# Optimization experiments

Measured on AMD Instinct MI355X. Metric: run time of the kernel, lower is better.

Reference implementation:

```python
import jax, jax.numpy as jnp
import numpy as np

N, E = 20000, 100000          # nodes, edges
H = 64                        # node_hidden_dim (== node_input_dim)
EIN, EH = 16, 128             # edge_input_dim, edge_hidden_dim
STEPS = 3                     # num_steps


def setup_inputs() -> dict:
    key = jax.random.key(0)
    ks = jax.random.split(key, 10)
    s = 0.05
    return {
        "node_features": jax.random.normal(ks[0], (N, H), jnp.float32),
        "edge_attr": jax.random.normal(ks[1], (E, EIN), jnp.float32),
        "edge_index": jax.random.randint(ks[2], (2, E), 0, N),
        # mp_input: Linear(H, H)
        "mp_w": jax.random.normal(ks[3], (H, H), jnp.float32) * s,
        "mp_b": jnp.zeros((H,), jnp.float32),
        # message_layer: Linear(2H, H)
        "msg_w": jax.random.normal(ks[4], (H, 2 * H), jnp.float32) * s,
        "msg_b": jnp.zeros((H,), jnp.float32),
        # edge network: Linear(EIN, EH) -> ReLU -> Linear(EH, H*H)
        "e1_w": jax.random.normal(ks[5], (EH, EIN), jnp.float32) * s,
        "e1_b": jnp.zeros((EH,), jnp.float32),
        "e2_w": jax.random.normal(ks[6], (H * H, EH), jnp.float32) * s,
        "e2_b": jnp.zeros((H * H,), jnp.float32),
        # NNConv root weight and bias
        "root": jax.random.normal(ks[7], (H, H), jnp.float32) * s,
        "conv_b": jnp.zeros((H,), jnp.float32),
    }


def reference(node_features, edge_attr, edge_index,
              mp_w, mp_b, msg_w, msg_b,
              e1_w, e1_b, e2_w, e2_b, root, conv_b):
    src, dst = edge_index[0], edge_index[1]
    out = jax.nn.relu(node_features @ mp_w.T + mp_b)  # [N, H]
    # Edge-conditioned weight matrices; edge_attr is constant across steps so
    # the edge MLP output is identical each step -> compute once (same math).
    W_e = (jax.nn.relu(edge_attr @ e1_w.T + e1_b) @ e2_w.T + e2_b).reshape(E, H, H)
    for _ in range(STEPS):
        # gather src features, per-edge matmul, scatter-add to dst
        msgs = jnp.einsum('ei,eio->eo', out[src], W_e)          # [E, H]
        agg = jax.ops.segment_sum(msgs, dst, num_segments=N)    # [N, H]
        m = jax.nn.relu(agg + out @ root + conv_b)              # NNConv + ReLU
        out = jnp.concatenate([m, out], axis=1) @ msg_w.T + msg_b
    return out + node_features
```

## Files before the change

kernel.cpp:

```cpp
#include <hip/hip_runtime.h>

#define N_ 20000
#define E_ 100000

typedef __attribute__((ext_vector_type(8))) short short8;
typedef __attribute__((ext_vector_type(8))) unsigned short ushort8;
typedef __attribute__((ext_vector_type(4))) float f32x4;

__device__ __forceinline__ unsigned short f2bf(float f) {
  union { float f; unsigned u; } v; v.f = f;
  unsigned r = v.u + 0x7fffu + ((v.u >> 16) & 1u);
  return (unsigned short)(r >> 16);
}
__device__ __forceinline__ float bf2f(unsigned short h) {
  union { unsigned u; float f; } v; v.u = ((unsigned)h) << 16;
  return v.f;
}

__global__ __launch_bounds__(256) void k_h2(const float* __restrict__ ea,
                                            const float* __restrict__ e1w,
                                            const float* __restrict__ e1b,
                                            unsigned short* __restrict__ h2) {
  int id = blockIdx.x * 256 + threadIdx.x;
  int e = id >> 7, k = id & 127;
  if (e >= E_) return;
  const float4* ar = (const float4*)(ea + e * 16);
  const float4* wr = (const float4*)(e1w + k * 16);
  float acc = e1b[k];
#pragma unroll
  for (int q = 0; q < 4; ++q) {
    float4 a = ar[q], w = wr[q];
    acc += a.x * w.x + a.y * w.y + a.z * w.z + a.w * w.w;
  }
  h2[id] = f2bf(fmaxf(acc, 0.f));
}

__global__ __launch_bounds__(256) void k_prep_bf(const float* __restrict__ e2w,
                                                 unsigned short* __restrict__ Bf) {
  int tid = blockIdx.x * 256 + threadIdx.x;
  int l = tid & 63, cf = (tid >> 6) & 255, kf = tid >> 14;
  int g = l >> 4, lm = l & 15;
  const float* src = e2w + (cf * 16 + lm) * 128 + kf * 32 + g * 8;
  float4 s0 = *(const float4*)(src);
  float4 s1 = *(const float4*)(src + 4);
  ushort8 v;
  v[0] = f2bf(s0.x); v[1] = f2bf(s0.y); v[2] = f2bf(s0.z); v[3] = f2bf(s0.w);
  v[4] = f2bf(s1.x); v[5] = f2bf(s1.y); v[6] = f2bf(s1.z); v[7] = f2bf(s1.w);
  *(ushort8*)(Bf + (size_t)tid * 8) = v;
}

__global__ __launch_bounds__(256) void k_node_in(const float* __restrict__ nfm,
                                                 const float* __restrict__ mpw,
                                                 const float* __restrict__ mpb,
                                                 const float* __restrict__ e2b,
                                                 float* __restrict__ outc,
                                                 float* __restrict__ yc) {
  __shared__ float wT[64 * 65];
  __shared__ float xr[4 * 65];
  __shared__ float nr[4 * 65];
  int t = threadIdx.x;
  for (int idx = t; idx < 4096; idx += 256) {
    int o = idx >> 6, i = idx & 63;
    wT[i * 65 + o] = mpw[idx];
  }
  __syncthreads();
  int nl = t >> 6, o = t & 63;
  for (int it = 0; it < 4; ++it) {
    int n = blockIdx.x * 16 + it * 4 + nl;
    xr[nl * 65 + o] = nfm[n * 64 + o];
    __syncthreads();
    float acc = mpb[o];
#pragma unroll 8
    for (int i = 0; i < 64; ++i) acc += xr[nl * 65 + i] * wT[i * 65 + o];
    float m = fmaxf(acc, 0.f);
    outc[n * 64 + o] = m;
    nr[nl * 65 + o] = m;
    __syncthreads();
    float yv = 0.f;
#pragma unroll 8
    for (int j = 0; j < 64; ++j) yv += nr[nl * 65 + j] * e2b[j * 64 + o];
    yc[n * 64 + o] = yv;
    __syncthreads();
  }
}

__global__ void k_zero(float* __restrict__ p, int n) {
  int i = blockIdx.x * 256 + threadIdx.x;
  if (i < n) p[i] = 0.f;
}

__global__ __launch_bounds__(256, 2) void k_msgs(const float* __restrict__ x,
                                                 const float* __restrict__ y,
                                                 const unsigned short* __restrict__ h2,
                                                 const unsigned short* __restrict__ Bf,
                                                 const int* __restrict__ ei,
                                                 float* __restrict__ agg) {
  __shared__ float xT[64 * 65];
  __shared__ unsigned short pm[4][64 * 66];
  __shared__ int sidx[64];
  __shared__ int didx[64];
  int t = threadIdx.x, w = t >> 6, l = t & 63;
  int e0 = blockIdx.x * 64;
  if (t < 64) {
    int e = e0 + t;
    sidx[t] = (e < E_) ? ei[e] : 0;
    didx[t] = (e < E_) ? ei[E_ + e] : -1;
  }
  __syncthreads();
  for (int it = 0; it < 16; ++it) {
    int idx = it * 256 + t;
    int e = idx >> 6, i = idx & 63;
    xT[i * 65 + e] = x[sidx[e] * 64 + i];
  }
  int g = l >> 4, lm = l & 15;
  short8 af[4][4];
#pragma unroll
  for (int mf = 0; mf < 4; ++mf) {
    int e = e0 + mf * 16 + lm;
    if (e >= E_) e = E_ - 1;
    const short8* hp = (const short8*)(h2 + (size_t)e * 128 + g * 8);
    af[mf][0] = hp[0]; af[mf][1] = hp[4]; af[mf][2] = hp[8]; af[mf][3] = hp[12];
  }
  __syncthreads();
  f32x4 macc[4][4];
#pragma unroll
  for (int mf = 0; mf < 4; ++mf)
#pragma unroll
    for (int nf = 0; nf < 4; ++nf) macc[mf][nf] = f32x4{0.f, 0.f, 0.f, 0.f};

  for (int il = 0; il < 16; ++il) {
    int i = w * 16 + il;
    f32x4 dacc[4][4];
#pragma unroll
    for (int mf = 0; mf < 4; ++mf)
#pragma unroll
      for (int nf = 0; nf < 4; ++nf) dacc[mf][nf] = f32x4{0.f, 0.f, 0.f, 0.f};
    const short8* bp = (const short8*)Bf + (i * 4) * 64 + l;
#pragma unroll
    for (int kf = 0; kf < 4; ++kf) {
      short8 b0 = bp[kf * 16384 + 0];
      short8 b1 = bp[kf * 16384 + 64];
      short8 b2 = bp[kf * 16384 + 128];
      short8 b3 = bp[kf * 16384 + 192];
#pragma unroll
      for (int mf = 0; mf < 4; ++mf) {
        dacc[mf][0] = __builtin_amdgcn_mfma_f32_16x16x32_bf16(af[mf][kf], b0, dacc[mf][0], 0, 0, 0);
        dacc[mf][1] = __builtin_amdgcn_mfma_f32_16x16x32_bf16(af[mf][kf], b1, dacc[mf][1], 0, 0, 0);
        dacc[mf][2] = __builtin_amdgcn_mfma_f32_16x16x32_bf16(af[mf][kf], b2, dacc[mf][2], 0, 0, 0);
        dacc[mf][3] = __builtin_amdgcn_mfma_f32_16x16x32_bf16(af[mf][kf], b3, dacc[mf][3], 0, 0, 0);
      }
    }
#pragma unroll
    for (int mf = 0; mf < 4; ++mf) {
      float xs0 = xT[i * 65 + mf * 16 + g * 4 + 0];
      float xs1 = xT[i * 65 + mf * 16 + g * 4 + 1];
      float xs2 = xT[i * 65 + mf * 16 + g * 4 + 2];
      float xs3 = xT[i * 65 + mf * 16 + g * 4 + 3];
#pragma unroll
      for (int nf = 0; nf < 4; ++nf) {
        macc[mf][nf][0] += xs0 * dacc[mf][nf][0];
        macc[mf][nf][1] += xs1 * dacc[mf][nf][1];
        macc[mf][nf][2] += xs2 * dacc[mf][nf][2];
        macc[mf][nf][3] += xs3 * dacc[mf][nf][3];
      }
    }
  }
#pragma unroll
  for (int mf = 0; mf < 4; ++mf)
#pragma unroll
    for (int nf = 0; nf < 4; ++nf)
#pragma unroll
      for (int r = 0; r < 4; ++r) {
        int e = mf * 16 + g * 4 + r, o = nf * 16 + lm;
        pm[w][e * 66 + o] = f2bf(macc[mf][nf][r]);
      }
  __syncthreads();
  for (int it = 0; it < 16; ++it) {
    int idx = it * 256 + t;
    int e = idx >> 6, o = idx & 63;
    int d = didx[e];
    if (d >= 0) {
      float v = bf2f(pm[0][e * 66 + o]) + bf2f(pm[1][e * 66 + o]) +
                bf2f(pm[2][e * 66 + o]) + bf2f(pm[3][e * 66 + o]);
      v += y[sidx[e] * 64 + o];
      atomicAdd(agg + (size_t)d * 64 + o, v);
    }
  }
}

__global__ __launch_bounds__(256) void k_update(const float* __restrict__ outc,
                                                const float* __restrict__ agg,
                                                const float* __restrict__ root,
                                                const float* __restrict__ convb,
                                                const float* __restrict__ msgw,
                                                const float* __restrict__ msgb,
                                                const float* __restrict__ e2b,
                                                const float* __restrict__ nfm,
                                                int last,
                                                float* __restrict__ outn,
                                                float* __restrict__ yn,
                                                float* __restrict__ dout) {
  __shared__ float wT[128 * 65];
  __shared__ float xr[4 * 65];
  __shared__ float mr[4 * 65];
  __shared__ float nr[4 * 65];
  int t = threadIdx.x;
  for (int idx = t; idx < 8192; idx += 256) {
    int o = idx >> 7, j = idx & 127;
    wT[j * 65 + o] = msgw[idx];
  }
  __syncthreads();
  int nl = t >> 6, o = t & 63;
  for (int it = 0; it < 4; ++it) {
    int n = blockIdx.x * 16 + it * 4 + nl;
    xr[nl * 65 + o] = outc[n * 64 + o];
    __syncthreads();
    float acc = agg[n * 64 + o] + convb[o];
#pragma unroll 8
    for (int i = 0; i < 64; ++i) acc += xr[nl * 65 + i] * root[i * 64 + o];
    float m = fmaxf(acc, 0.f);
    mr[nl * 65 + o] = m;
    __syncthreads();
    float o2 = msgb[o];
#pragma unroll 8
    for (int j = 0; j < 64; ++j)
      o2 += mr[nl * 65 + j] * wT[j * 65 + o] + xr[nl * 65 + j] * wT[(64 + j) * 65 + o];
    nr[nl * 65 + o] = o2;
    __syncthreads();
    if (last) {
      dout[n * 64 + o] = o2 + nfm[n * 64 + o];
    } else {
      float yv = 0.f;
#pragma unroll 8
      for (int j = 0; j < 64; ++j) yv += nr[nl * 65 + j] * e2b[j * 64 + o];
      outn[n * 64 + o] = o2;
      yn[n * 64 + o] = yv;
    }
    __syncthreads();
  }
}

extern "C" void kernel_launch(void* const* d_in, const int* in_sizes, int n_in,
                              void* d_out, int out_size, void* d_ws, size_t ws_size,
                              hipStream_t stream) {
  const float* nfm  = (const float*)d_in[0];
  const float* ea   = (const float*)d_in[1];
  const int*   ei   = (const int*)d_in[2];
  const float* mpw  = (const float*)d_in[3];
  const float* mpb  = (const float*)d_in[4];
  const float* msgw = (const float*)d_in[5];
  const float* msgb = (const float*)d_in[6];
  const float* e1w  = (const float*)d_in[7];
  const float* e1b  = (const float*)d_in[8];
  const float* e2w  = (const float*)d_in[9];
  const float* e2b  = (const float*)d_in[10];
  const float* root = (const float*)d_in[11];
  const float* convb= (const float*)d_in[12];
  float* out = (float*)d_out;

  char* ws = (char*)d_ws;
  unsigned short* h2 = (unsigned short*)ws; ws += (size_t)E_ * 128 * 2;
  unsigned short* Bf = (unsigned short*)ws; ws += (size_t)4096 * 128 * 2;
  float* outa = (float*)ws; ws += (size_t)N_ * 64 * 4;
  float* ya   = (float*)ws; ws += (size_t)N_ * 64 * 4;
  float* outb = (float*)ws; ws += (size_t)N_ * 64 * 4;
  float* yb   = (float*)ws; ws += (size_t)N_ * 64 * 4;
  float* agg  = (float*)ws; ws += (size_t)N_ * 64 * 4;

  hipLaunchKernelGGL(k_prep_bf, dim3(256), dim3(256), 0, stream, e2w, Bf);
  hipLaunchKernelGGL(k_h2, dim3((E_ * 128) / 256), dim3(256), 0, stream, ea, e1w, e1b, h2);
  hipLaunchKernelGGL(k_node_in, dim3(N_ / 16), dim3(256), 0, stream, nfm, mpw, mpb, e2b, outa, ya);

  float* oc = outa; float* yc = ya; float* on = outb; float* yv = yb;
  for (int s = 0; s < 3; ++s) {
    hipLaunchKernelGGL(k_zero, dim3((N_ * 64 + 255) / 256), dim3(256), 0, stream, agg, N_ * 64);
    hipLaunchKernelGGL(k_msgs, dim3((E_ + 63) / 64), dim3(256), 0, stream, oc, yc, h2, Bf, ei, agg);
    hipLaunchKernelGGL(k_update, dim3(N_ / 16), dim3(256), 0, stream, oc, agg, root, convb,
                       msgw, msgb, e2b, nfm, (s == 2) ? 1 : 0, on, yv, out);
    float* tp;
    tp = oc; oc = on; on = tp;
    tp = yc; yc = yv; yv = tp;
  }
}
```

Before: 734.3 us.

## Swap MFMA operand roles in k_msgs, MFMA edge MLP, fuse agg zeroing

The per-edge message kernel now treats the weight tiles as the A operand and the per-edge hidden vectors as B. This lets each wave chain four K-steps per output quarter directly, with no separate partial-accumulator arrays, which lowers register pressure and allows raising occupancy to 3 blocks per CU. The first edge-MLP layer is recomputed with MFMA, folding the bias in through an extra ones column. Zeroing of the aggregation buffer moves into k_update so two of the per-step zero launches disappear. The trade-off is an extra global write in the update kernel and a different output layout that must stay consistent with the pm transpose.

New measurement: 916.4 us. 24.8% more time.

```diff
diff --git a/kernel.cpp b/kernel.cpp
--- a/kernel.cpp
+++ b/kernel.cpp
@@ -16,37 +16,64 @@
   union { unsigned u; float f; } v; v.u = ((unsigned)h) << 16;
   return v.f;
 }
+__device__ __forceinline__ short8 pack8(float4 a, float4 b) {
+  short8 v;
+  v[0] = (short)f2bf(a.x); v[1] = (short)f2bf(a.y);
+  v[2] = (short)f2bf(a.z); v[3] = (short)f2bf(a.w);
+  v[4] = (short)f2bf(b.x); v[5] = (short)f2bf(b.y);
+  v[6] = (short)f2bf(b.z); v[7] = (short)f2bf(b.w);
+  return v;
+}
 
 __global__ __launch_bounds__(256) void k_h2(const float* __restrict__ ea,
                                             const float* __restrict__ e1w,
                                             const float* __restrict__ e1b,
                                             unsigned short* __restrict__ h2) {
-  int id = blockIdx.x * 256 + threadIdx.x;
-  int e = id >> 7, k = id & 127;
-  if (e >= E_) return;
-  const float4* ar = (const float4*)(ea + e * 16);
-  const float4* wr = (const float4*)(e1w + k * 16);
-  float acc = e1b[k];
-#pragma unroll
-  for (int q = 0; q < 4; ++q) {
-    float4 a = ar[q], w = wr[q];
-    acc += a.x * w.x + a.y * w.y + a.z * w.z + a.w * w.w;
-  }
-  h2[id] = f2bf(fmaxf(acc, 0.f));
+  int t = threadIdx.x, w = t >> 6, l = t & 63, g = l >> 4, lm = l & 15;
+  int e0 = blockIdx.x * 64 + w * 16;
+  short8 bf[8];
+#pragma unroll
+  for (int cf = 0; cf < 8; ++cf) {
+    int c = cf * 16 + lm;
+    short8 v = {0, 0, 0, 0, 0, 0, 0, 0};
+    if (g < 2) {
+      const float4* wp = (const float4*)(e1w + c * 16 + g * 8);
+      v = pack8(wp[0], wp[1]);
+    } else if (g == 2) {
+      v[0] = (short)f2bf(e1b[c]);
+    }
+    bf[cf] = v;
+  }
+  int er = e0 + lm; if (er >= E_) er = E_ - 1;
+  short8 a = {0, 0, 0, 0, 0, 0, 0, 0};
+  if (g < 2) {
+    const float4* ap = (const float4*)(ea + er * 16 + g * 8);
+    a = pack8(ap[0], ap[1]);
+  } else if (g == 2) {
+    a[0] = (short)0x3F80;
+  }
+  f32x4 z = {0.f, 0.f, 0.f, 0.f};
+#pragma unroll
+  for (int cf = 0; cf < 8; ++cf) {
+    f32x4 acc = __builtin_amdgcn_mfma_f32_16x16x32_bf16(a, bf[cf], z, 0, 0, 0);
+#pragma unroll
+    for (int r = 0; r < 4; ++r) {
+      int e = e0 + g * 4 + r;
+      if (e < E_) h2[(size_t)e * 128 + cf * 16 + lm] = f2bf(fmaxf(acc[r], 0.f));
+    }
+  }
 }
 
 __global__ __launch_bounds__(256) void k_prep_bf(const float* __restrict__ e2w,
-                                                 unsigned short* __restrict__ Bf) {
+                                                 unsigned short* __restrict__ Af) {
   int tid = blockIdx.x * 256 + threadIdx.x;
   int l = tid & 63, cf = (tid >> 6) & 255, kf = tid >> 14;
   int g = l >> 4, lm = l & 15;
   const float* src = e2w + (cf * 16 + lm) * 128 + kf * 32 + g * 8;
   float4 s0 = *(const float4*)(src);
   float4 s1 = *(const float4*)(src + 4);
-  ushort8 v;
-  v[0] = f2bf(s0.x); v[1] = f2bf(s0.y); v[2] = f2bf(s0.z); v[3] = f2bf(s0.w);
-  v[4] = f2bf(s1.x); v[5] = f2bf(s1.y); v[6] = f2bf(s1.z); v[7] = f2bf(s1.w);
-  *(ushort8*)(Bf + (size_t)tid * 8) = v;
+  short8 v = pack8(s0, s1);
+  *(short8*)((short*)Af + (size_t)tid * 8) = v;
 }
 
 __global__ __launch_bounds__(256) void k_node_in(const float* __restrict__ nfm,
@@ -89,90 +116,92 @@
   if (i < n) p[i] = 0.f;
 }
 
-__global__ __launch_bounds__(256, 2) void k_msgs(const float* __restrict__ x,
+__global__ __launch_bounds__(256, 3) void k_msgs(const float* __restrict__ x,
                                                  const float* __restrict__ y,
                                                  const unsigned short* __restrict__ h2,
-                                                 const unsigned short* __restrict__ Bf,
+                                                 const unsigned short* __restrict__ Af,
                                                  const int* __restrict__ ei,
                                                  float* __restrict__ agg) {
   __shared__ float xT[64 * 65];
   __shared__ unsigned short pm[4][64 * 66];
   __shared__ int sidx[64];
   __shared__ int didx[64];
-  int t = threadIdx.x, w = t >> 6, l = t & 63;
+  int t = threadIdx.x, w = t >> 6, l = t & 63, g = l >> 4, lm = l & 15;
   int e0 = blockIdx.x * 64;
   if (t < 64) {
     int e = e0 + t;
     sidx[t] = (e < E_) ? ei[e] : 0;
     didx[t] = (e < E_) ? ei[E_ + e] : -1;
   }
+  short8 hf[4][4];
+#pragma unroll
+  for (int ef = 0; ef < 4; ++ef) {
+    int e = e0 + ef * 16 + lm;
+    if (e >= E_) e = E_ - 1;
+    const short8* hp = (const short8*)(h2 + (size_t)e * 128 + g * 8);
+    hf[ef][0] = hp[0]; hf[ef][1] = hp[4]; hf[ef][2] = hp[8]; hf[ef][3] = hp[12];
+  }
   __syncthreads();
   for (int it = 0; it < 16; ++it) {
     int idx = it * 256 + t;
     int e = idx >> 6, i = idx & 63;
-    xT[i * 65 + e] = x[sidx[e] * 64 + i];
-  }
-  int g = l >> 4, lm = l & 15;
-  short8 af[4][4];
-#pragma unroll
-  for (int mf = 0; mf < 4; ++mf) {
-    int e = e0 + mf * 16 + lm;
-    if (e >= E_) e = E_ - 1;
-    const short8* hp = (const short8*)(h2 + (size_t)e * 128 + g * 8);
-    af[mf][0] = hp[0]; af[mf][1] = hp[4]; af[mf][2] = hp[8]; af[mf][3] = hp[12];
-  }
-  __syncthreads();
+    xT[i * 65 + e] = x[(size_t)sidx[e] * 64 + i];
+  }
+  __syncthreads();
+
   f32x4 macc[4][4];
 #pragma unroll
-  for (int mf = 0; mf < 4; ++mf)
-#pragma unroll
-    for (int nf = 0; nf < 4; ++nf) macc[mf][nf] = f32x4{0.f, 0.f, 0.f, 0.f};
+  for (int ef = 0; ef < 4; ++ef)
+#pragma unroll
+    for (int oq = 0; oq < 4; ++oq) macc[ef][oq] = f32x4{0.f, 0.f, 0.f, 0.f};
+  f32x4 z = {0.f, 0.f, 0.f, 0.f};
+  const short8* As = (const short8*)Af;
 
   for (int il = 0; il < 16; ++il) {
     int i = w * 16 + il;
-    f32x4 dacc[4][4];
-#pragma unroll
-    for (int mf = 0; mf < 4; ++mf)
-#pragma unroll
-      for (int nf = 0; nf < 4; ++nf) dacc[mf][nf] = f32x4{0.f, 0.f, 0.f, 0.f};
-    const short8* bp = (const short8*)Bf + (i * 4) * 64 + l;
-#pragma unroll
-    for (int kf = 0; kf < 4; ++kf) {
-      short8 b0 = bp[kf * 16384 + 0];
-      short8 b1 = bp[kf * 16384 + 64];
-      short8 b2 = bp[kf * 16384 + 128];
-      short8 b3 = bp[kf * 16384 + 192];
-#pragma unroll
-      for (int mf = 0; mf < 4; ++mf) {
-        dacc[mf][0] = __builtin_amdgcn_mfma_f32_16x16x32_bf16(af[mf][kf], b0, dacc[mf][0], 0, 0, 0);
-        dacc[mf][1] = __builtin_amdgcn_mfma_f32_16x16x32_bf16(af[mf][kf], b1, dacc[mf][1], 0, 0, 0);
-        dacc[mf][2] = __builtin_amdgcn_mfma_f32_16x16x32_bf16(af[mf][kf], b2, dacc[mf][2], 0, 0, 0);
-        dacc[mf][3] = __builtin_amdgcn_mfma_f32_16x16x32_bf16(af[mf][kf], b3, dacc[mf][3], 0, 0, 0);
-      }
-    }
-#pragma unroll
-    for (int mf = 0; mf < 4; ++mf) {
-      float xs0 = xT[i * 65 + mf * 16 + g * 4 + 0];
-      float xs1 = xT[i * 65 + mf * 16 + g * 4 + 1];
-      float xs2 = xT[i * 65 + mf * 16 + g * 4 + 2];
-      float xs3 = xT[i * 65 + mf * 16 + g * 4 + 3];
-#pragma unroll
-      for (int nf = 0; nf < 4; ++nf) {
-        macc[mf][nf][0] += xs0 * dacc[mf][nf][0];
-        macc[mf][nf][1] += xs1 * dacc[mf][nf][1];
-        macc[mf][nf][2] += xs2 * dacc[mf][nf][2];
-        macc[mf][nf][3] += xs3 * dacc[mf][nf][3];
-      }
-    }
-  }
-#pragma unroll
-  for (int mf = 0; mf < 4; ++mf)
-#pragma unroll
-    for (int nf = 0; nf < 4; ++nf)
+    float xs0 = xT[i * 65 + 0 + lm];
+    float xs1 = xT[i * 65 + 16 + lm];
+    float xs2 = xT[i * 65 + 32 + lm];
+    float xs3 = xT[i * 65 + 48 + lm];
+#pragma unroll
+    for (int oq = 0; oq < 4; ++oq) {
+      int ct = i * 4 + oq;
+      const short8* ap = As + ct * 64 + l;
+      short8 a0 = ap[0];
+      short8 a1 = ap[16384];
+      short8 a2 = ap[32768];
+      short8 a3 = ap[49152];
+      f32x4 d0, d1, d2, d3;
+      d0 = __builtin_amdgcn_mfma_f32_16x16x32_bf16(a0, hf[0][0], z, 0, 0, 0);
+      d1 = __builtin_amdgcn_mfma_f32_16x16x32_bf16(a0, hf[1][0], z, 0, 0, 0);
+      d2 = __builtin_amdgcn_mfma_f32_16x16x32_bf16(a0, hf[2][0], z, 0, 0, 0);
+      d3 = __builtin_amdgcn_mfma_f32_16x16x32_bf16(a0, hf[3][0], z, 0, 0, 0);
+      d0 = __builtin_amdgcn_mfma_f32_16x16x32_bf16(a1, hf[0][1], d0, 0, 0, 0);
+      d1 = __builtin_amdgcn_mfma_f32_16x16x32_bf16(a1, hf[1][1], d1, 0, 0, 0);
+      d2 = __builtin_amdgcn_mfma_f32_16x16x32_bf16(a1, hf[2][1], d2, 0, 0, 0);
+      d3 = __builtin_amdgcn_mfma_f32_16x16x32_bf16(a1, hf[3][1], d3, 0, 0, 0);
+      d0 = __builtin_amdgcn_mfma_f32_16x16x32_bf16(a2, hf[0][2], d0, 0, 0, 0);
+      d1 = __builtin_amdgcn_mfma_f32_16x16x32_bf16(a2, hf[1][2], d1, 0, 0, 0);
+      d2 = __builtin_amdgcn_mfma_f32_16x16x32_bf16(a2, hf[2][2], d2, 0, 0, 0);
+      d3 = __builtin_amdgcn_mfma_f32_16x16x32_bf16(a2, hf[3][2], d3, 0, 0, 0);
+      d0 = __builtin_amdgcn_mfma_f32_16x16x32_bf16(a3, hf[0][3], d0, 0, 0, 0);
+      d1 = __builtin_amdgcn_mfma_f32_16x16x32_bf16(a3, hf[1][3], d1, 0, 0, 0);
+      d2 = __builtin_amdgcn_mfma_f32_16x16x32_bf16(a3, hf[2][3], d2, 0, 0, 0);
+      d3 = __builtin_amdgcn_mfma_f32_16x16x32_bf16(a3, hf[3][3], d3, 0, 0, 0);
+      macc[0][oq] += xs0 * d0;
+      macc[1][oq] += xs1 * d1;
+      macc[2][oq] += xs2 * d2;
+      macc[3][oq] += xs3 * d3;
+    }
+  }
+#pragma unroll
+  for (int ef = 0; ef < 4; ++ef)
+#pragma unroll
+    for (int oq = 0; oq < 4; ++oq)
 #pragma unroll
       for (int r = 0; r < 4; ++r) {
-        int e = mf * 16 + g * 4 + r, o = nf * 16 + lm;
-        pm[w][e * 66 + o] = f2bf(macc[mf][nf][r]);
+        int e = ef * 16 + lm, o = oq * 16 + g * 4 + r;
+        pm[w][e * 66 + o] = f2bf(macc[ef][oq][r]);
       }
   __syncthreads();
   for (int it = 0; it < 16; ++it) {
@@ -182,14 +211,14 @@
     if (d >= 0) {
       float v = bf2f(pm[0][e * 66 + o]) + bf2f(pm[1][e * 66 + o]) +
                 bf2f(pm[2][e * 66 + o]) + bf2f(pm[3][e * 66 + o]);
-      v += y[sidx[e] * 64 + o];
+      v += y[(size_t)sidx[e] * 64 + o];
       atomicAdd(agg + (size_t)d * 64 + o, v);
     }
   }
 }
 
 __global__ __launch_bounds__(256) void k_update(const float* __restrict__ outc,
-                                                const float* __restrict__ agg,
+                                                float* __restrict__ agg,
                                                 const float* __restrict__ root,
                                                 const float* __restrict__ convb,
                                                 const float* __restrict__ msgw,
@@ -216,6 +245,7 @@
     xr[nl * 65 + o] = outc[n * 64 + o];
     __syncthreads();
     float acc = agg[n * 64 + o] + convb[o];
+    agg[n * 64 + o] = 0.f;
 #pragma unroll 8
     for (int i = 0; i < 64; ++i) acc += xr[nl * 65 + i] * root[i * 64 + o];
     float m = fmaxf(acc, 0.f);
@@ -260,21 +290,21 @@
 
   char* ws = (char*)d_ws;
   unsigned short* h2 = (unsigned short*)ws; ws += (size_t)E_ * 128 * 2;
-  unsigned short* Bf = (unsigned short*)ws; ws += (size_t)4096 * 128 * 2;
+  unsigned short* Af = (unsigned short*)ws; ws += (size_t)4096 * 128 * 2;
   float* outa = (float*)ws; ws += (size_t)N_ * 64 * 4;
   float* ya   = (float*)ws; ws += (size_t)N_ * 64 * 4;
   float* outb = (float*)ws; ws += (size_t)N_ * 64 * 4;
   float* yb   = (float*)ws; ws += (size_t)N_ * 64 * 4;
   float* agg  = (float*)ws; ws += (size_t)N_ * 64 * 4;
 
-  hipLaunchKernelGGL(k_prep_bf, dim3(256), dim3(256), 0, stream, e2w, Bf);
-  hipLaunchKernelGGL(k_h2, dim3((E_ * 128) / 256), dim3(256), 0, stream, ea, e1w, e1b, h2);
+  hipLaunchKernelGGL(k_prep_bf, dim3(256), dim3(256), 0, stream, e2w, Af);
+  hipLaunchKernelGGL(k_zero, dim3((N_ * 64 + 255) / 256), dim3(256), 0, stream, agg, N_ * 64);
+  hipLaunchKernelGGL(k_h2, dim3((E_ + 63) / 64), dim3(256), 0, stream, ea, e1w, e1b, h2);
   hipLaunchKernelGGL(k_node_in, dim3(N_ / 16), dim3(256), 0, stream, nfm, mpw, mpb, e2b, outa, ya);
 
   float* oc = outa; float* yc = ya; float* on = outb; float* yv = yb;
   for (int s = 0; s < 3; ++s) {
-    hipLaunchKernelGGL(k_zero, dim3((N_ * 64 + 255) / 256), dim3(256), 0, stream, agg, N_ * 64);
-    hipLaunchKernelGGL(k_msgs, dim3((E_ + 63) / 64), dim3(256), 0, stream, oc, yc, h2, Bf, ei, agg);
+    hipLaunchKernelGGL(k_msgs, dim3((E_ + 63) / 64), dim3(256), 0, stream, oc, yc, h2, Af, ei, agg);
     hipLaunchKernelGGL(k_update, dim3(N_ / 16), dim3(256), 0, stream, oc, agg, root, convb,
                        msgw, msgb, e2b, nfm, (s == 2) ? 1 : 0, on, yv, out);
     float* tp;
```
